# Kernel tuning notes

Hardware: AMD Instinct MI355X
Metric: run time of the kernel (lower is better)

## Reference

```python
import jax, jax.numpy as jnp
import numpy as np

C = 768; H = 12; D = C // H; R = 8; SCALE = 0.5; EPS = 1e-12
NEG = -1e9

def _lin(x, W, b):
    return x @ W + b

def _ln(x, g, b):
    m = jnp.mean(x, axis=-1, keepdims=True)
    v = jnp.mean((x - m) ** 2, axis=-1, keepdims=True)
    return (x - m) * jax.lax.rsqrt(v + EPS) * g + b

def setup_inputs() -> dict:
    key = jax.random.key(0)
    ks = jax.random.split(key, 16)
    B, T, K = 8, 512, 4
    s = 0.02
    inp = {
        'x': jax.random.normal(ks[0], (B, T, C), jnp.float32),
        'mask': jnp.ones((B, T), jnp.int32),
        'neighbour_rep': jax.random.normal(ks[1], (B, T - 1, K, C), jnp.float32),
        'Wq': jax.random.normal(ks[2], (C, C), jnp.float32) * s,
        'bq': jnp.zeros((C,), jnp.float32),
        'Wk': jax.random.normal(ks[3], (C, C), jnp.float32) * s,
        'bk': jnp.zeros((C,), jnp.float32),
        'Wv': jax.random.normal(ks[4], (C, C), jnp.float32) * s,
        'bv': jnp.zeros((C,), jnp.float32),
        'Wp': jax.random.normal(ks[5], (C, C), jnp.float32) * s,
        'bp': jnp.zeros((C,), jnp.float32),
        'Wd': jax.random.normal(ks[6], (C, R), jnp.float32) * s,
        'bd': jnp.zeros((R,), jnp.float32),
        'Wu': jax.random.normal(ks[7], (R, C), jnp.float32) * s,
        'bu': jnp.zeros((C,), jnp.float32),
        'ln_g': jnp.ones((C,), jnp.float32),
        'ln_b': jnp.zeros((C,), jnp.float32),
    }
    return inp

def _softmax_stable(att):
    # manual max-sub-exp-sum softmax, matching stable_softmax
    att = att - jnp.max(att, axis=-1, keepdims=True)
    att = jnp.exp(att)
    return att / jnp.sum(att, axis=-1, keepdims=True)

def _heads(t, n_tok):
    B = t.shape[0]
    return t.reshape(B, n_tok, H, D)

def reference(x, mask, neighbour_rep, Wq, bq, Wk, bk, Wv, bv, Wp, bp, Wd, bd, Wu, bu, ln_g, ln_b):
    B, T, _ = x.shape
    inv = 1.0 / jnp.sqrt(jnp.float32(D))
    mvalid = (mask != 0)[:, None, None, :]  # [B,1,1,T]

    # ---- self attention: queries are x[:,1:], keys/values over full seq ----
    q = _heads(_lin(x[:, 1:], Wq, bq), T - 1)      # [B,T-1,H,D]
    k = _heads(_lin(x, Wk, bk), T)                 # [B,T,H,D]
    v = _heads(_lin(x, Wv, bv), T)
    att = jnp.einsum('bqhd,bkhd->bhqk', q, k) * inv
    att = jnp.where(mvalid, att, NEG)
    att = _softmax_stable(att)
    y_self = jnp.einsum('bhqk,bkhd->bqhd', att, v).reshape(B, T - 1, C)
    y_self = _lin(y_self, Wp, bp)

    # ---- cls attention: single query (token 0), low-rank key projection ----
    qc = _heads(_lin(x[:, :1], Wq, bq), 1)                         # [B,1,H,D]
    kc = _heads(_lin(_lin(x, Wd, bd), Wu, bu), T)                  # [B,T,H,D]
    attc = jnp.einsum('bqhd,bkhd->bhqk', qc, kc) * inv
    attc = jnp.where(mvalid, attc, NEG)
    attc = _softmax_stable(attc)
    y_cls = jnp.einsum('bhqk,bkhd->bqhd', attc, v).reshape(B, 1, C)
    y_cls = _lin(y_cls, Wp, bp)

    # ---- neighbour attention over small candidate set per token ----
    cand = jnp.concatenate([x[:, 1:, None, :], neighbour_rep], axis=2)  # [B,T-1,Kc,C]
    Kc = cand.shape[2]
    qn = _lin(cand, Wq, bq).reshape(B, T - 1, Kc, H, D)
    kn = _lin(_lin(cand, Wd, bd), Wu, bu).reshape(B, T - 1, Kc, H, D)
    vn = _lin(cand, Wv, bv).reshape(B, T - 1, Kc, H, D)
    attn = jnp.einsum('btihd,btjhd->bthij', qn, kn) * inv
    attn = _softmax_stable(attn)
    out = jnp.einsum('bthij,btjhd->btihd', attn, vn).reshape(B, T - 1, Kc, C)
    out = _lin(out, Wp, bp)
    y_neigh = out[:, :, 0, :]
    neigh_tmp = out[:, :, 1:, :]

    y = SCALE * y_neigh + (1.0 - SCALE) * y_self
    neighbour_out = _ln(neigh_tmp + neighbour_rep, ln_g, ln_b)
    y = jnp.concatenate([y_cls, y], axis=1)
    y = _ln(y + x, ln_g, ln_b)
    return y, neighbour_out
```

## Files before the change

### kernel.cpp

```cpp
#include <hip/hip_runtime.h>
#include <math.h>

#define C_    768
#define H_    12
#define D_    64
#define B_    8
#define T_    512
#define TM1   511
#define R_    8
#define KN_   4
#define KC5   5
#define SCALE_ 0.5f
#define EPS_  1e-12f
#define NEG_  -1000000000.0f
#define INV_  0.125f
#define LDQ   2432
#define QPOFF 2304
#define LDVQ  896
#define NT_   4096
#define NRR_  16352

typedef __bf16 bf16_t;
typedef __bf16 bf16x4_t __attribute__((ext_vector_type(4)));
typedef __bf16 bf16x8_t __attribute__((ext_vector_type(8)));
typedef float  f32x4_t  __attribute__((ext_vector_type(4)));
typedef const void __attribute__((address_space(1)))* gas_t;
typedef void       __attribute__((address_space(3)))* las_t;

__device__ __forceinline__ void gl_lds16(const bf16_t* g, bf16_t* l) {
  __builtin_amdgcn_global_load_lds((gas_t)g, (las_t)l, 16, 0, 0);
}

__device__ __forceinline__ int swz(int row, int g) {
  return row * 32 + (((g ^ (row >> 1)) & 3) << 3);
}

struct GemmDesc {
  const bf16_t* A; int lda;
  const bf16_t* Bt;
  const float* bias;
  bf16_t* Cbf; int ldc;
  bf16_t* Ctr; int trcol0; int mode;
  int M, K, N, gx, nwg;
};

__global__ __launch_bounds__(256) void prep(
    const float* __restrict__ x, const float* __restrict__ nrep,
    const float* __restrict__ Wq, const float* __restrict__ Wk,
    const float* __restrict__ Wv, const float* __restrict__ Wp,
    const float* __restrict__ Wd, const float* __restrict__ Wu,
    const float* __restrict__ bq, const float* __restrict__ bk,
    const float* __restrict__ bv, const float* __restrict__ bu,
    const float* __restrict__ bp,
    bf16_t* __restrict__ xbf, bf16_t* __restrict__ nrbf,
    bf16_t* __restrict__ Wbig, bf16_t* __restrict__ Wtp,
    bf16_t* __restrict__ Wvbf,
    float* __restrict__ WdT, float* __restrict__ bbig,
    float* __restrict__ zb768)
{
  __shared__ float tile[32][33];
  const int bid = blockIdx.x, tid = threadIdx.x;
  if (bid < 1024) {
    const long n = (long)NT_ * C_;
    for (long i = ((long)bid * 256 + tid) * 4; i < n; i += (long)1024 * 256 * 4) {
      float4 v = *(const float4*)(x + i);
      bf16x4_t o = {(bf16_t)v.x, (bf16_t)v.y, (bf16_t)v.z, (bf16_t)v.w};
      *(bf16x4_t*)(xbf + i) = o;
    }
  } else if (bid < 3072) {
    const long n = (long)NRR_ * C_;
    for (long i = ((long)(bid - 1024) * 256 + tid) * 4; i < n;
         i += (long)2048 * 256 * 4) {
      float4 v = *(const float4*)(nrep + i);
      bf16x4_t o = {(bf16_t)v.x, (bf16_t)v.y, (bf16_t)v.z, (bf16_t)v.w};
      *(bf16x4_t*)(nrbf + i) = o;
    }
  } else if (bid < 5376) {
    int sub = bid - 3072;
    const int which = sub / 576; sub %= 576;
    if (which == 2) {
      const long i = ((long)sub * 256 + tid) * 4;
      float4 v = *(const float4*)(Wv + i);
      bf16x4_t o = {(bf16_t)v.x, (bf16_t)v.y, (bf16_t)v.z, (bf16_t)v.w};
      *(bf16x4_t*)(Wvbf + i) = o;
    } else {
      const float* W = which == 0 ? Wq : which == 1 ? Wk : Wp;
      bf16_t* Wt = (which == 3) ? Wtp : Wbig + (size_t)which * C_ * C_;
      const int n0 = (sub % 24) * 32, k0 = (sub / 24) * 32;
      const int tx = tid & 31, ty = tid >> 5;
      #pragma unroll
      for (int r = ty; r < 32; r += 8)
        tile[r][tx] = W[(size_t)(k0 + r) * C_ + n0 + tx];
      __syncthreads();
      #pragma unroll
      for (int r = ty; r < 32; r += 8)
        Wt[(size_t)(n0 + r) * C_ + k0 + tx] = (bf16_t)tile[tx][r];
    }
  } else if (bid < 5760) {
    const int idx = (bid - 5376) * 256 + tid;
    const int n = idx / C_, k = idx % C_;
    const int h = n / 10, r = n % 10;
    float s = 0.f;
    if (h < H_ && r < 9) {
      if (r < 8) {
        #pragma unroll 8
        for (int j = 0; j < 64; ++j)
          s += Wu[r * C_ + h * 64 + j] * Wq[(size_t)k * C_ + h * 64 + j];
      } else {
        #pragma unroll 8
        for (int j = 0; j < 64; ++j)
          s += bu[h * 64 + j] * Wq[(size_t)k * C_ + h * 64 + j];
      }
    }
    Wbig[(size_t)(QPOFF + n) * C_ + k] = (bf16_t)s;
  } else if (bid < 5784) {
    const int idx = (bid - 5760) * 256 + tid;
    if (idx < R_ * C_) {
      const int r = idx / C_, k = idx % C_;
      WdT[idx] = Wd[(size_t)k * R_ + r];
    }
  } else {
    const int i = (bid - 5784) * 256 + tid;
    if (i < LDQ) {
      float v;
      if (i < 768) v = bq[i];
      else if (i < 1536) v = bk[i - 768];
      else if (i < 2304) {
        const int n = i - 1536;
        float s = bp[n];
        for (int m = 0; m < C_; ++m) s += bv[m] * Wp[(size_t)m * C_ + n];
        v = s;
      } else {
        const int n = i - QPOFF, h = n / 10, r = n % 10;
        v = 0.f;
        if (h < H_ && r < 9) {
          if (r < 8) {
            float s = 0.f;
            for (int j = 0; j < 64; ++j) s += bq[h * 64 + j] * Wu[r * C_ + h * 64 + j];
            v = s;
          } else {
            float s = 0.f;
            for (int j = 0; j < 64; ++j) s += bq[h * 64 + j] * bu[h * 64 + j];
            v = s;
          }
        }
      }
      bbig[i] = v;
    } else if (i < LDQ + 768) {
      zb768[i - LDQ] = 0.f;
    }
  }
}

__device__ __forceinline__ void gemm_body(const GemmDesc& d, int bid0, char* pool)
{
  bf16_t* Cs = (bf16_t*)pool;

  int lid = bid0;
  {
    const int nwg = d.nwg;
    const int q0 = nwg >> 3, r0 = nwg & 7;
    const int xcd = lid & 7, idx = lid >> 3;
    lid = (xcd < r0 ? xcd * (q0 + 1) : r0 * (q0 + 1) + (xcd - r0) * q0) + idx;
  }
  const int row0 = (lid / d.gx) * 128;
  const int col0 = (lid % d.gx) * 128;

  const int tid = threadIdx.x;
  const int lane = tid & 63;
  const int wv = tid >> 6;
  const int wr = (wv >> 1) * 64;
  const int wc = (wv & 1) * 64;
  const int wvo = wv * 512;

  const int sr = tid >> 2;
  const int ssl = (tid & 3) ^ ((sr >> 1) & 3);
  const int sk = ssl * 8;

  int ra0 = row0 + sr;       if (ra0 > d.M - 1) ra0 = d.M - 1;
  int ra1 = row0 + 64 + sr;  if (ra1 > d.M - 1) ra1 = d.M - 1;
  const bf16_t* ga0 = d.A + (size_t)ra0 * d.lda + sk;
  const bf16_t* ga1 = d.A + (size_t)ra1 * d.lda + sk;
  const bf16_t* gb0 = d.Bt + (size_t)(col0 + sr) * d.K + sk;
  const bf16_t* gb1 = d.Bt + (size_t)(col0 + 64 + sr) * d.K + sk;

  f32x4_t acc[4][4];
  #pragma unroll
  for (int i = 0; i < 4; ++i)
    #pragma unroll
    for (int j = 0; j < 4; ++j) acc[i][j] = (f32x4_t){0.f, 0.f, 0.f, 0.f};

  const int fm = lane & 15;
  const int g = lane >> 4;

  {
    bf16_t* a0 = (bf16_t*)pool;
    bf16_t* b0 = (bf16_t*)(pool + 8192);
    gl_lds16(ga0, a0 + wvo);
    gl_lds16(ga1, a0 + 2048 + wvo);
    gl_lds16(gb0, b0 + wvo);
    gl_lds16(gb1, b0 + 2048 + wvo);
  }
  __syncthreads();

  unsigned cur = 0;
  for (int k0 = 32; k0 < d.K; k0 += 32) {
    {
      char* nb = pool + ((cur ^ 1u) << 14);
      bf16_t* na = (bf16_t*)nb;
      bf16_t* nbb = (bf16_t*)(nb + 8192);
      gl_lds16(ga0 + k0, na + wvo);
      gl_lds16(ga1 + k0, na + 2048 + wvo);
      gl_lds16(gb0 + k0, nbb + wvo);
      gl_lds16(gb1 + k0, nbb + 2048 + wvo);
    }
    {
      const bf16_t* cA = (const bf16_t*)(pool + (cur << 14));
      const bf16_t* cB = (const bf16_t*)(pool + (cur << 14) + 8192);
      bf16x8_t af[4], bfr[4];
      #pragma unroll
      for (int mi = 0; mi < 4; ++mi)
        af[mi] = *(const bf16x8_t*)(cA + swz(wr + mi * 16 + fm, g));
      #pragma unroll
      for (int ni = 0; ni < 4; ++ni)
        bfr[ni] = *(const bf16x8_t*)(cB + swz(wc + ni * 16 + fm, g));
      __builtin_amdgcn_s_setprio(1);
      #pragma unroll
      for (int mi = 0; mi < 4; ++mi)
        #pragma unroll
        for (int ni = 0; ni < 4; ++ni)
          acc[mi][ni] = __builtin_amdgcn_mfma_f32_16x16x32_bf16(af[mi], bfr[ni],
                                                                acc[mi][ni], 0, 0, 0);
      __builtin_amdgcn_s_setprio(0);
    }
    __syncthreads();
    cur ^= 1u;
  }
  {
    const bf16_t* cA = (const bf16_t*)(pool + (cur << 14));
    const bf16_t* cB = (const bf16_t*)(pool + (cur << 14) + 8192);
    bf16x8_t af[4], bfr[4];
    #pragma unroll
    for (int mi = 0; mi < 4; ++mi)
      af[mi] = *(const bf16x8_t*)(cA + swz(wr + mi * 16 + fm, g));
    #pragma unroll
    for (int ni = 0; ni < 4; ++ni)
      bfr[ni] = *(const bf16x8_t*)(cB + swz(wc + ni * 16 + fm, g));
    __builtin_amdgcn_s_setprio(1);
    #pragma unroll
    for (int mi = 0; mi < 4; ++mi)
      #pragma unroll
      for (int ni = 0; ni < 4; ++ni)
        acc[mi][ni] = __builtin_amdgcn_mfma_f32_16x16x32_bf16(af[mi], bfr[ni],
                                                              acc[mi][ni], 0, 0, 0);
    __builtin_amdgcn_s_setprio(0);
  }
  __syncthreads();

  const int r4 = (lane >> 4) * 4;

  if (d.mode & 2) {
    #pragma unroll
    for (int ni = 0; ni < 4; ++ni) {
      const int col = col0 + wc + ni * 16 + fm;
      if ((unsigned)(col - d.trcol0) < 768u) {
        const int vcol = col - d.trcol0;
        const float bv = d.bias[col];
        #pragma unroll
        for (int mi = 0; mi < 4; ++mi) {
          const int rb = row0 + wr + mi * 16 + r4;
          bf16x4_t o4 = {(bf16_t)(acc[mi][ni][0] + bv), (bf16_t)(acc[mi][ni][1] + bv),
                         (bf16_t)(acc[mi][ni][2] + bv), (bf16_t)(acc[mi][ni][3] + bv)};
          size_t idx = ((size_t)(rb >> 9) * H_ + (size_t)(vcol >> 6)) * ((size_t)D_ * T_)
                     + (size_t)(vcol & 63) * T_ + (size_t)(rb & 511);
          *(bf16x4_t*)(d.Ctr + idx) = o4;
        }
      }
    }
  }

  #pragma unroll
  for (int p = 0; p < 2; ++p) {
    if (wr == p * 64) {
      #pragma unroll
      for (int ni = 0; ni < 4; ++ni) {
        const int col = wc + ni * 16 + fm;
        const float bv = d.bias[col0 + col];
        #pragma unroll
        for (int mi = 0; mi < 4; ++mi) {
          const int lrow = mi * 16 + r4;
          #pragma unroll
          for (int r = 0; r < 4; ++r)
            Cs[(lrow + r) * 136 + col] = (bf16_t)(acc[mi][ni][r] + bv);
        }
      }
    }
    __syncthreads();
    const int rrow = tid >> 2;
    const int cc = (tid & 3) * 32;
    const int grow = row0 + p * 64 + rrow;
    if ((d.mode & 1) && grow < d.M) {
      bf16_t* gp = d.Cbf + (size_t)grow * d.ldc + col0 + cc;
      const bf16_t* lp = Cs + rrow * 136 + cc;
      #pragma unroll
      for (int j = 0; j < 4; ++j)
        *(bf16x8_t*)(gp + j * 8) = *(const bf16x8_t*)(lp + j * 8);
    }
    __syncthreads();
  }
}

__device__ __forceinline__ void gemv8w_body(
    const bf16_t* __restrict__ A, const float* __restrict__ WdT,
    const float* __restrict__ bd, float* __restrict__ out, int M, int bid)
{
  const int w = (int)threadIdx.x >> 6, lane = (int)threadIdx.x & 63;
  const int row0 = bid * 16 + w * 4;
  #pragma unroll
  for (int rr = 0; rr < 4; ++rr) {
    const int row = row0 + rr;
    if (row >= M) return;
    const bf16_t* ar = A + (size_t)row * C_ + lane * 12;
    float xv[12];
    #pragma unroll
    for (int c = 0; c < 3; ++c) {
      bf16x4_t v = *(const bf16x4_t*)(ar + c * 4);
      #pragma unroll
      for (int j = 0; j < 4; ++j) xv[c * 4 + j] = (float)v[j];
    }
    float acc[8];
    #pragma unroll
    for (int r = 0; r < 8; ++r) {
      const float* wr = WdT + r * C_ + lane * 12;
      float4 w0 = *(const float4*)(wr);
      float4 w1 = *(const float4*)(wr + 4);
      float4 w2 = *(const float4*)(wr + 8);
      acc[r] = xv[0]*w0.x + xv[1]*w0.y + xv[2]*w0.z + xv[3]*w0.w
             + xv[4]*w1.x + xv[5]*w1.y + xv[6]*w1.z + xv[7]*w1.w
             + xv[8]*w2.x + xv[9]*w2.y + xv[10]*w2.z + xv[11]*w2.w;
    }
    #pragma unroll
    for (int off = 32; off > 0; off >>= 1) {
      #pragma unroll
      for (int r = 0; r < 8; ++r) acc[r] += __shfl_xor(acc[r], off);
    }
    if (lane == 0) {
      #pragma unroll
      for (int r = 0; r < 8; ++r)
        out[(size_t)row * R_ + r] = acc[r] + bd[r];
    }
  }
}

__global__ __launch_bounds__(256) void mega1(
    GemmDesc d0, int n0, GemmDesc d1, int n1,
    const bf16_t* Ag1, const bf16_t* Ag2,
    const float* WdT, const float* bd,
    float* o1, int M1, int ng1, float* o2, int M2)
{
  __shared__ __align__(16) char pool[32768];
  int bid = blockIdx.x;
  if (bid < n0) { gemm_body(d0, bid, pool); return; }
  bid -= n0;
  if (bid < n1) { gemm_body(d1, bid, pool); return; }
  bid -= n1;
  if (bid < ng1) { gemv8w_body(Ag1, WdT, bd, o1, M1, bid); return; }
  bid -= ng1;
  gemv8w_body(Ag2, WdT, bd, o2, M2, bid);
}

__global__ __launch_bounds__(256) void gemm_mfma_k(GemmDesc d) {
  __shared__ __align__(16) char pool[32768];
  gemm_body(d, blockIdx.x, pool);
}

__device__ void attn_body(
    const bf16_t* __restrict__ QKVc, const bf16_t* __restrict__ Vtg,
    const int* __restrict__ mask, bf16_t* __restrict__ yout,
    char* pool, int bid)
{
  bf16_t* Ks   = (bf16_t*)pool;
  bf16_t* Vs   = (bf16_t*)(pool + 8192);
  bf16_t* Pl   = (bf16_t*)(pool + 16384);
  float* fac_s = (float*)(pool + 24576);
  float* l_s   = (float*)(pool + 24832);
  int*   msk_s = (int*)(pool + 25088);

  const int qt0 = (bid & 7) * 64;
  const int h = (bid >> 3) % H_;
  const int b = bid / 96;
  const int tid = threadIdx.x;
  const int lane = tid & 63;
  const int w = tid >> 6;
  const int lq = lane & 15;
  const int g = lane >> 4;

  const int qi_frag = qt0 + w * 16 + lq;
  const int qtok = (qi_frag < TM1 ? qi_frag : TM1 - 1) + 1;
  bf16x8_t qf[2];
  {
    const bf16_t* qp = QKVc + ((size_t)(b * T_) + qtok) * LDQ + h * D_ + 8 * g;
    qf[0] = *(const bf16x8_t*)qp;
    qf[1] = *(const bf16x8_t*)(qp + 32);
  }

  const bf16_t* kbase = QKVc + (size_t)(b * T_) * LDQ + 768 + h * D_;
  const bf16_t* vbase = Vtg + ((size_t)(b * H_) + h) * ((size_t)D_ * T_);

  f32x4_t o[4];
  #pragma unroll
  for (int i = 0; i < 4; ++i) o[i] = (f32x4_t){0.f, 0.f, 0.f, 0.f};
  float m = -INFINITY, l = 0.f;

  for (int kt = 0; kt < T_; kt += 64) {
    #pragma unroll
    for (int i = 0; i < 2; ++i) {
      const int tp = tid + i * 256;
      const int kr = tp >> 3;
      const int sl = tp & 7;
      const int ss = sl ^ (kr & 7);
      gl_lds16(kbase + (size_t)(kt + kr) * LDQ + 8 * ss,
               Ks + (size_t)(i * 4 + w) * 512);
      gl_lds16(vbase + (size_t)kr * T_ + kt + 8 * ss,
               Vs + (size_t)(i * 4 + w) * 512);
    }
    if (tid < 64) msk_s[tid] = mask[b * T_ + kt + tid];
    __syncthreads();

    f32x4_t st[4];
    __builtin_amdgcn_s_setprio(1);
    #pragma unroll
    for (int t = 0; t < 4; ++t) {
      st[t] = (f32x4_t){0.f, 0.f, 0.f, 0.f};
      const int kk = t * 16 + lq;
      const bf16_t* krow = Ks + kk * 64;
      bf16x8_t kf0 = *(const bf16x8_t*)(krow + 8 * ((g)     ^ (kk & 7)));
      bf16x8_t kf1 = *(const bf16x8_t*)(krow + 8 * ((4 + g) ^ (kk & 7)));
      st[t] = __builtin_amdgcn_mfma_f32_16x16x32_bf16(kf0, qf[0], st[t], 0, 0, 0);
      st[t] = __builtin_amdgcn_mfma_f32_16x16x32_bf16(kf1, qf[1], st[t], 0, 0, 0);
    }
    __builtin_amdgcn_s_setprio(0);

    float p[16];
    float mt = -INFINITY;
    #pragma unroll
    for (int t = 0; t < 4; ++t) {
      const int4 mk = *(const int4*)&msk_s[t * 16 + 4 * g];
      p[4*t+0] = mk.x ? st[t][0] * INV_ : NEG_;
      p[4*t+1] = mk.y ? st[t][1] * INV_ : NEG_;
      p[4*t+2] = mk.z ? st[t][2] * INV_ : NEG_;
      p[4*t+3] = mk.w ? st[t][3] * INV_ : NEG_;
      mt = fmaxf(mt, fmaxf(fmaxf(p[4*t], p[4*t+1]), fmaxf(p[4*t+2], p[4*t+3])));
    }
    mt = fmaxf(mt, __shfl_xor(mt, 16));
    mt = fmaxf(mt, __shfl_xor(mt, 32));
    const float mnew = fmaxf(m, mt);
    const float fac = __expf(m - mnew);
    float ps = 0.f;
    #pragma unroll
    for (int i = 0; i < 16; ++i) { p[i] = __expf(p[i] - mnew); ps += p[i]; }
    ps += __shfl_xor(ps, 16);
    ps += __shfl_xor(ps, 32);
    l = l * fac + ps;
    m = mnew;
    if (lane < 16) fac_s[w * 16 + lane] = fac;

    bf16_t* prow = Pl + w * 1024 + lq * 64;
    #pragma unroll
    for (int t = 0; t < 4; ++t) {
      bf16x4_t pb = {(bf16_t)p[4*t], (bf16_t)p[4*t+1],
                     (bf16_t)p[4*t+2], (bf16_t)p[4*t+3]};
      *(bf16x4_t*)(prow + 8 * ((2*t + (g >> 1)) ^ (lq & 7)) + 4 * (g & 1)) = pb;
    }
    bf16x8_t pa0 = *(const bf16x8_t*)(prow + 8 * ((g)     ^ (lq & 7)));
    bf16x8_t pa1 = *(const bf16x8_t*)(prow + 8 * ((4 + g) ^ (lq & 7)));

    const float4 fc = *(const float4*)&fac_s[w * 16 + 4 * g];
    __builtin_amdgcn_s_setprio(1);
    #pragma unroll
    for (int db = 0; db < 4; ++db) {
      const int dr = db * 16 + lq;
      const bf16_t* vrow = Vs + dr * 64;
      bf16x8_t vf0 = *(const bf16x8_t*)(vrow + 8 * ((g)     ^ (dr & 7)));
      bf16x8_t vf1 = *(const bf16x8_t*)(vrow + 8 * ((4 + g) ^ (dr & 7)));
      o[db][0] *= fc.x; o[db][1] *= fc.y; o[db][2] *= fc.z; o[db][3] *= fc.w;
      o[db] = __builtin_amdgcn_mfma_f32_16x16x32_bf16(pa0, vf0, o[db], 0, 0, 0);
      o[db] = __builtin_amdgcn_mfma_f32_16x16x32_bf16(pa1, vf1, o[db], 0, 0, 0);
    }
    __builtin_amdgcn_s_setprio(0);
    __syncthreads();
  }

  if (lane < 16) l_s[w * 16 + lane] = l;
  const float4 lv = *(const float4*)&l_s[w * 16 + 4 * g];
  const float rl0 = 1.f / lv.x, rl1 = 1.f / lv.y;
  const float rl2 = 1.f / lv.z, rl3 = 1.f / lv.w;
  const int qr0 = qt0 + w * 16 + 4 * g;
  #pragma unroll
  for (int db = 0; db < 4; ++db) {
    const int col = h * D_ + db * 16 + lq;
    bf16_t* yp = yout + ((size_t)(b * TM1) + qr0) * C_ + col;
    if (qr0 + 0 < TM1) yp[0 * (size_t)C_] = (bf16_t)(o[db][0] * rl0);
    if (qr0 + 1 < TM1) yp[1 * (size_t)C_] = (bf16_t)(o[db][1] * rl1);
    if (qr0 + 2 < TM1) yp[2 * (size_t)C_] = (bf16_t)(o[db][2] * rl2);
    if (qr0 + 3 < TM1) yp[3 * (size_t)C_] = (bf16_t)(o[db][3] * rl3);
  }
}

__device__ void cls_body(
    const bf16_t* __restrict__ QKVc, const float* __restrict__ t1,
    const int* __restrict__ mask, float* __restrict__ ycp,
    char* pool, int cbid)
{
  float* Vs   = (float*)pool;
  float* Ps   = (float*)(pool + 16640);
  float* qp_s = (float*)(pool + 16960);

  const int b = cbid / H_, h = cbid % H_;
  const int tid = threadIdx.x;
  const int lane = tid & 63;

  if (tid < 9)
    qp_s[tid] = (float)QKVc[(size_t)(b * T_) * LDQ + QPOFF + h * 10 + tid];
  __syncthreads();

  float m = -INFINITY, l = 0.f, acc = 0.f, mnew = 0.f;
  for (int kt = 0; kt < T_; kt += 64) {
    for (int rr = tid >> 6; rr < 64; rr += 4)
      Vs[rr * 65 + lane] =
          (float)QKVc[((size_t)(b * T_) + kt + rr) * LDQ + 1536 + h * D_ + lane];
    __syncthreads();
    if (tid < 64) {
      const float* t1r = t1 + ((size_t)(b * T_) + kt + tid) * R_;
      float sc = qp_s[8];
      #pragma unroll
      for (int r = 0; r < 8; ++r) sc += qp_s[r] * t1r[r];
      sc *= INV_;
      if (!mask[b * T_ + kt + tid]) sc = NEG_;
      float mt = sc;
      #pragma unroll
      for (int off = 32; off > 0; off >>= 1) mt = fmaxf(mt, __shfl_xor(mt, off));
      mnew = fmaxf(m, mt);
      float e = __expf(sc - mnew);
      float ssum = e;
      #pragma unroll
      for (int off = 32; off > 0; off >>= 1) ssum += __shfl_xor(ssum, off);
      float fac = __expf(m - mnew);
      acc *= fac;
      l = l * fac + ssum;
      Ps[tid] = e;
    }
    __syncthreads();
    if (tid < 64) {
      #pragma unroll
      for (int j = 0; j < 64; ++j) acc += Ps[j] * Vs[j * 65 + tid];
      m = mnew;
    }
    __syncthreads();
  }
  if (tid < 64) ycp[(size_t)b * C_ + h * D_ + tid] = acc / l;
}

__global__ __launch_bounds__(256) void attn_cls(
    const bf16_t* __restrict__ QKVc, const bf16_t* __restrict__ Vtg,
    const int* __restrict__ mask, bf16_t* __restrict__ yout,
    const float* __restrict__ t1, float* __restrict__ ycp)
{
  __shared__ __align__(16) char pool[25344];
  const int bid = blockIdx.x;
  if (bid < 768) attn_body(QKVc, Vtg, mask, yout, pool, bid);
  else           cls_body(QKVc, t1, mask, ycp, pool, bid - 768);
}

__global__ __launch_bounds__(256) void neigh_attn(
    const bf16_t* __restrict__ QKVc, const float* __restrict__ t1,
    const bf16_t* __restrict__ vqn, const float* __restrict__ t2,
    const bf16_t* __restrict__ ysp, int b0, bf16_t* __restrict__ poutn)
{
  __shared__ float vs[KC5 * C_];
  __shared__ float qp_s[KC5][128];
  __shared__ float t2_s[KC5][8];
  __shared__ float Ps[H_ * 25];

  const int tid = threadIdx.x;
  const int bt = blockIdx.x;
  const int bb = bt / TM1, t = bt % TM1;
  const int b = b0 + bb;
  const size_t tok = (size_t)(b * T_) + t + 1;
  const size_t nrow = ((size_t)(bb * TM1) + t) * KN_;

  for (int idx = tid; idx < KC5 * 96; idx += 256) {
    int i = idx / 96, d8 = (idx % 96) * 8;
    const bf16_t* vp = (i == 0) ? QKVc + tok * LDQ + 1536 + d8
                                : vqn + (nrow + i - 1) * LDVQ + d8;
    bf16x8_t vv = *(const bf16x8_t*)vp;
    #pragma unroll
    for (int j = 0; j < 8; ++j) vs[i * C_ + d8 + j] = (float)vv[j];
  }
  for (int idx = tid; idx < KC5 * 16; idx += 256) {
    int i = idx / 16, c8 = (idx % 16) * 8;
    const bf16_t* qpp = (i == 0) ? QKVc + tok * LDQ + QPOFF + c8
                                 : vqn + (nrow + i - 1) * LDVQ + 768 + c8;
    bf16x8_t qv = *(const bf16x8_t*)qpp;
    #pragma unroll
    for (int j = 0; j < 8; ++j) qp_s[i][c8 + j] = (float)qv[j];
  }
  if (tid < KC5 * 8) {
    int i = tid / 8, r = tid & 7;
    t2_s[i][r] = (i == 0) ? t1[tok * R_ + r] : t2[(nrow + i - 1) * R_ + r];
  }
  __syncthreads();

  if (tid < H_ * KC5) {
    int h = tid / KC5, i = tid % KC5;
    float sc[KC5];
    #pragma unroll
    for (int j = 0; j < KC5; ++j) {
      float s = qp_s[i][h * 10 + 8];
      #pragma unroll
      for (int r = 0; r < 8; ++r) s += qp_s[i][h * 10 + r] * t2_s[j][r];
      sc[j] = s * INV_;
    }
    float mt = sc[0];
    #pragma unroll
    for (int j = 1; j < KC5; ++j) mt = fmaxf(mt, sc[j]);
    float e[KC5], ssum = 0.f;
    #pragma unroll
    for (int j = 0; j < KC5; ++j) { e[j] = __expf(sc[j] - mt); ssum += e[j]; }
    float rs = 1.f / ssum;
    #pragma unroll
    for (int j = 0; j < KC5; ++j) Ps[h * 25 + i * KC5 + j] = e[j] * rs;
  }
  __syncthreads();

  const bf16_t* ysrow = ysp + ((size_t)(b * TM1) + t) * C_;
  for (int idx = tid; idx < KC5 * C_; idx += 256) {
    int i = idx / C_, c = idx % C_;
    int h = c / D_;
    float sum = 0.f;
    #pragma unroll
    for (int j = 0; j < KC5; ++j)
      sum += Ps[h * 25 + i * KC5 + j] * vs[j * C_ + c];
    if (i == 0) sum = SCALE_ * sum + (1.f - SCALE_) * (float)ysrow[c];
    poutn[(((size_t)(bb * TM1) + t) * KC5 + i) * C_ + c] = (bf16_t)sum;
  }
}

__device__ __forceinline__ void block_reduce2(float& s, float& ss, float* red) {
  #pragma unroll
  for (int off = 32; off > 0; off >>= 1) {
    s += __shfl_down(s, off);
    ss += __shfl_down(ss, off);
  }
  int wid = threadIdx.x >> 6;
  if ((threadIdx.x & 63) == 0) { red[wid * 2] = s; red[wid * 2 + 1] = ss; }
  __syncthreads();
  s  = red[0] + red[2] + red[4] + red[6];
  ss = red[1] + red[3] + red[5] + red[7];
}

__device__ __forceinline__ void ln_row(const float vals[3], float s, float ss,
                                       const float* __restrict__ g,
                                       const float* __restrict__ bb,
                                       float* __restrict__ orow, float* red) {
  block_reduce2(s, ss, red);
  float mean = s * (1.f / (float)C_);
  float var = ss * (1.f / (float)C_) - mean * mean;
  var = fmaxf(var, 0.f);
  float rs = rsqrtf(var + EPS_);
  #pragma unroll
  for (int ii = 0; ii < 3; ++ii) {
    int c = threadIdx.x + ii * 256;
    orow[c] = (vals[ii] - mean) * rs * g[c] + bb[c];
  }
}

__global__ __launch_bounds__(256) void combine_all(
    const bf16_t* __restrict__ poutnb, const float* __restrict__ x,
    const float* __restrict__ g, const float* __restrict__ bln,
    int b0, float* __restrict__ dout, float* __restrict__ dout1,
    const bf16_t* __restrict__ nrcbf, int nMain,
    const float* __restrict__ ycp)
{
  __shared__ float red[8];
  int bid = blockIdx.x;
  float vals[3], s = 0.f, ss = 0.f;
  if (bid < nMain) {
    const int bbb = bid / TM1, t = bid % TM1;
    const int b = b0 + bbb;
    const bf16_t* pn = poutnb + (((size_t)(bbb * TM1) + t) * KC5 + 0) * C_;
    const float* xr = x + ((size_t)(b * T_) + t + 1) * C_;
    float* orow = dout + ((size_t)(b * T_) + t + 1) * C_;
    #pragma unroll
    for (int ii = 0; ii < 3; ++ii) {
      int c = threadIdx.x + ii * 256;
      float v = (float)pn[c] + xr[c];
      vals[ii] = v; s += v; ss += v * v;
    }
    ln_row(vals, s, ss, g, bln, orow, red);
    return;
  }
  bid -= nMain;
  if (bid < nMain * KN_) {
    const int i1 = bid % KN_;
    const int bt = bid / KN_;
    const int bbb = bt / TM1, t = bt % TM1;
    const int b = b0 + bbb;
    const bf16_t* pn = poutnb + ((size_t)bt * KC5 + 1 + i1) * C_;
    const bf16_t* nr = nrcbf + ((size_t)bt * KN_ + i1) * C_;
    float* orow = dout1 + (((size_t)(b * TM1) + t) * KN_ + i1) * C_;
    #pragma unroll
    for (int ii = 0; ii < 3; ++ii) {
      int c = threadIdx.x + ii * 256;
      float v = (float)pn[c] + (float)nr[c];
      vals[ii] = v; s += v; ss += v * v;
    }
    ln_row(vals, s, ss, g, bln, orow, red);
    return;
  }
  bid -= nMain * KN_;
  const int b = bid;
  const float* yc = ycp + (size_t)b * C_;
  const float* xr = x + (size_t)(b * T_) * C_;
  float* orow = dout + (size_t)(b * T_) * C_;
  #pragma unroll
  for (int ii = 0; ii < 3; ++ii) {
    int c = threadIdx.x + ii * 256;
    float v = yc[c] + xr[c];
    vals[ii] = v; s += v; ss += v * v;
  }
  ln_row(vals, s, ss, g, bln, orow, red);
}

extern "C" void kernel_launch(void* const* d_in, const int* in_sizes, int n_in,
                              void* d_out, int out_size, void* d_ws, size_t ws_size,
                              hipStream_t stream) {
  (void)in_sizes; (void)n_in; (void)out_size;
  const float* x    = (const float*)d_in[0];
  const int*   mask = (const int*)d_in[1];
  const float* nrep = (const float*)d_in[2];
  const float* Wq = (const float*)d_in[3];  const float* bq = (const float*)d_in[4];
  const float* Wk = (const float*)d_in[5];  const float* bk = (const float*)d_in[6];
  const float* Wv = (const float*)d_in[7];  const float* bv = (const float*)d_in[8];
  const float* Wp = (const float*)d_in[9];  const float* bp = (const float*)d_in[10];
  const float* Wd = (const float*)d_in[11]; const float* bd = (const float*)d_in[12];
  const float* Wu = (const float*)d_in[13]; const float* bu = (const float*)d_in[14];
  const float* lng = (const float*)d_in[15];
  const float* lnb = (const float*)d_in[16];
  float* dout = (float*)d_out;
  const size_t OUT1 = (size_t)B_ * T_ * C_;

  char* ws = (char*)d_ws;
  size_t off = 0;
  auto alloc = [&](size_t bytes) -> void* {
    void* p = ws + off; off += (bytes + 255) & ~(size_t)255; return p;
  };
  const size_t NT = (size_t)NT_;
  const size_t NR = (size_t)NRR_;
  const size_t YSROWS = (size_t)B_ * TM1;

  bf16_t* xbf   = (bf16_t*)alloc(NT * C_ * 2);
  bf16_t* nrbf  = (bf16_t*)alloc(NR * C_ * 2);
  bf16_t* Wbig  = (bf16_t*)alloc((size_t)LDQ * C_ * 2);
  bf16_t* Wtp   = (bf16_t*)alloc((size_t)C_ * C_ * 2);
  bf16_t* Wvbf  = (bf16_t*)alloc((size_t)C_ * C_ * 2);
  float*  WdT   = (float*)alloc((size_t)R_ * C_ * 4);
  float*  bbig  = (float*)alloc(LDQ * 4);
  float*  zb768 = (float*)alloc(768 * 4);
  bf16_t* QKVc  = (bf16_t*)alloc(NT * LDQ * 2);
  bf16_t* Vtg   = (bf16_t*)alloc(NT * C_ * 2);
  float*  t1    = (float*)alloc(NT * R_ * 4);
  bf16_t* ysp   = (bf16_t*)alloc(YSROWS * C_ * 2);
  float*  ycp   = (float*)alloc((size_t)B_ * C_ * 4);
  const size_t fixed = off;
  const size_t perb = (size_t)TM1 * KN_ * LDVQ * 2
                    + (size_t)TM1 * KN_ * R_ * 4
                    + (size_t)TM1 * KC5 * C_ * 2 + 4 * 256;
  int nb = 1;
  for (int cand : {8, 4, 2, 1}) {
    if (fixed + perb * (size_t)cand <= ws_size) { nb = cand; break; }
  }
  bf16_t* poutnb = (bf16_t*)alloc((size_t)nb * TM1 * KC5 * C_ * 2);
  bf16_t* vqn  = (bf16_t*)alloc((size_t)nb * TM1 * KN_ * LDVQ * 2);
  float*  t2   = (float*)alloc((size_t)nb * TM1 * KN_ * R_ * 4);

  dim3 blk(256);

  prep<<<5797, blk, 0, stream>>>(x, nrep, Wq, Wk, Wv, Wp, Wd, Wu,
                                 bq, bk, bv, bu, bp,
                                 xbf, nrbf, Wbig, Wtp, Wvbf, WdT, bbig, zb768);

  GemmDesc dwvp;
  dwvp.A = Wtp; dwvp.lda = C_; dwvp.Bt = Wvbf; dwvp.bias = zb768;
  dwvp.Cbf = Wbig + (size_t)1536 * C_; dwvp.ldc = C_;
  dwvp.Ctr = nullptr; dwvp.trcol0 = 0; dwvp.mode = 1;
  dwvp.M = C_; dwvp.K = C_; dwvp.N = C_; dwvp.gx = 6; dwvp.nwg = 36;
  gemm_mfma_k<<<36, blk, 0, stream>>>(dwvp);

  GemmDesc dqkv;
  dqkv.A = xbf; dqkv.lda = C_; dqkv.Bt = Wbig; dqkv.bias = bbig;
  dqkv.Cbf = QKVc; dqkv.ldc = LDQ; dqkv.Ctr = Vtg; dqkv.trcol0 = 1536;
  dqkv.mode = 3; dqkv.M = (int)NT; dqkv.K = C_; dqkv.N = LDQ;
  dqkv.gx = LDQ / 128; dqkv.nwg = (LDQ / 128) * 32;

  bool first = true;
  for (int b0 = 0; b0 < B_; b0 += nb) {
    const int Mn = nb * TM1 * KN_;
    const bf16_t* nrcbf = nrbf + (size_t)b0 * TM1 * KN_ * C_;

    GemmDesc dvqn;
    dvqn.A = nrcbf; dvqn.lda = C_; dvqn.Bt = Wbig + (size_t)1536 * C_;
    dvqn.bias = bbig + 1536; dvqn.Cbf = vqn; dvqn.ldc = LDVQ;
    dvqn.Ctr = nullptr; dvqn.trcol0 = 0; dvqn.mode = 1;
    dvqn.M = Mn; dvqn.K = C_; dvqn.N = LDVQ;
    dvqn.gx = LDVQ / 128; dvqn.nwg = (LDVQ / 128) * ((Mn + 127) / 128);

    const int n0 = first ? dqkv.nwg : 0;
    const int M1 = first ? (int)NT : 0;
    const int ng1 = first ? (int)((NT + 15) / 16) : 0;
    const int ng2 = (Mn + 15) / 16;

    mega1<<<n0 + dvqn.nwg + ng1 + ng2, blk, 0, stream>>>(
        dqkv, n0, dvqn, dvqn.nwg, xbf, nrcbf, WdT, bd, t1, M1, ng1, t2, Mn);

    if (first) {
      attn_cls<<<768 + 96, blk, 0, stream>>>(QKVc, Vtg, mask, ysp, t1, ycp);
    }

    neigh_attn<<<nb * TM1, blk, 0, stream>>>(QKVc, t1, vqn, t2, ysp, b0, poutnb);

    combine_all<<<nb * TM1 * (1 + KN_) + (first ? 8 : 0), blk, 0, stream>>>(
        poutnb, x, lng, lnb, b0, dout, dout + OUT1, nrcbf, nb * TM1, ycp);

    first = false;
  }
}
```

Before: 236.8 us.

## Merge self/cls attention and neighbour attention into one launch

Fuses the attn_cls and neigh_attn kernels into a single attn_neigh launch that dispatches blocks by index range, sharing one shared-memory pool. To remove the dependency of neighbour attention on the self-attention output, the SCALE blend with y_self moves from neigh_attn into combine_all. This saves a kernel launch and lets the two attention workloads run concurrently. In exchange, neighbour blocks now use the larger 25 KB pool, which may lower their occupancy.

```diff
diff --git a/kernel.cpp b/kernel.cpp
--- a/kernel.cpp
+++ b/kernel.cpp
@@ -561,29 +561,17 @@
   if (tid < 64) ycp[(size_t)b * C_ + h * D_ + tid] = acc / l;
 }
 
-__global__ __launch_bounds__(256) void attn_cls(
-    const bf16_t* __restrict__ QKVc, const bf16_t* __restrict__ Vtg,
-    const int* __restrict__ mask, bf16_t* __restrict__ yout,
-    const float* __restrict__ t1, float* __restrict__ ycp)
-{
-  __shared__ __align__(16) char pool[25344];
-  const int bid = blockIdx.x;
-  if (bid < 768) attn_body(QKVc, Vtg, mask, yout, pool, bid);
-  else           cls_body(QKVc, t1, mask, ycp, pool, bid - 768);
-}
-
-__global__ __launch_bounds__(256) void neigh_attn(
+__device__ void neigh_body(
     const bf16_t* __restrict__ QKVc, const float* __restrict__ t1,
     const bf16_t* __restrict__ vqn, const float* __restrict__ t2,
-    const bf16_t* __restrict__ ysp, int b0, bf16_t* __restrict__ poutn)
+    int b0, bf16_t* __restrict__ poutn, char* pool, int bt)
 {
-  __shared__ float vs[KC5 * C_];
-  __shared__ float qp_s[KC5][128];
-  __shared__ float t2_s[KC5][8];
-  __shared__ float Ps[H_ * 25];
+  float* vs   = (float*)pool;
+  float* qp_s = (float*)(pool + 15360);
+  float* t2_s = (float*)(pool + 17920);
+  float* Ps   = (float*)(pool + 18080);
 
   const int tid = threadIdx.x;
-  const int bt = blockIdx.x;
   const int bb = bt / TM1, t = bt % TM1;
   const int b = b0 + bb;
   const size_t tok = (size_t)(b * T_) + t + 1;
@@ -603,11 +591,11 @@
                                  : vqn + (nrow + i - 1) * LDVQ + 768 + c8;
     bf16x8_t qv = *(const bf16x8_t*)qpp;
     #pragma unroll
-    for (int j = 0; j < 8; ++j) qp_s[i][c8 + j] = (float)qv[j];
+    for (int j = 0; j < 8; ++j) qp_s[i * 128 + c8 + j] = (float)qv[j];
   }
   if (tid < KC5 * 8) {
     int i = tid / 8, r = tid & 7;
-    t2_s[i][r] = (i == 0) ? t1[tok * R_ + r] : t2[(nrow + i - 1) * R_ + r];
+    t2_s[i * 8 + r] = (i == 0) ? t1[tok * R_ + r] : t2[(nrow + i - 1) * R_ + r];
   }
   __syncthreads();
 
@@ -616,9 +604,9 @@
     float sc[KC5];
     #pragma unroll
     for (int j = 0; j < KC5; ++j) {
-      float s = qp_s[i][h * 10 + 8];
-      #pragma unroll
-      for (int r = 0; r < 8; ++r) s += qp_s[i][h * 10 + r] * t2_s[j][r];
+      float s = qp_s[i * 128 + h * 10 + 8];
+      #pragma unroll
+      for (int r = 0; r < 8; ++r) s += qp_s[i * 128 + h * 10 + r] * t2_s[j * 8 + r];
       sc[j] = s * INV_;
     }
     float mt = sc[0];
@@ -633,7 +621,6 @@
   }
   __syncthreads();
 
-  const bf16_t* ysrow = ysp + ((size_t)(b * TM1) + t) * C_;
   for (int idx = tid; idx < KC5 * C_; idx += 256) {
     int i = idx / C_, c = idx % C_;
     int h = c / D_;
@@ -641,9 +628,25 @@
     #pragma unroll
     for (int j = 0; j < KC5; ++j)
       sum += Ps[h * 25 + i * KC5 + j] * vs[j * C_ + c];
-    if (i == 0) sum = SCALE_ * sum + (1.f - SCALE_) * (float)ysrow[c];
     poutn[(((size_t)(bb * TM1) + t) * KC5 + i) * C_ + c] = (bf16_t)sum;
   }
+}
+
+__global__ __launch_bounds__(256) void attn_neigh(
+    int nAttn, int nCls,
+    const bf16_t* __restrict__ QKVc, const bf16_t* __restrict__ Vtg,
+    const int* __restrict__ mask, bf16_t* __restrict__ ysp,
+    const float* __restrict__ t1, float* __restrict__ ycp,
+    const bf16_t* __restrict__ vqn, const float* __restrict__ t2,
+    int b0, bf16_t* __restrict__ poutn)
+{
+  __shared__ __align__(16) char pool[25344];
+  int bid = blockIdx.x;
+  if (bid < nAttn) { attn_body(QKVc, Vtg, mask, ysp, pool, bid); return; }
+  bid -= nAttn;
+  if (bid < nCls) { cls_body(QKVc, t1, mask, ycp, pool, bid); return; }
+  bid -= nCls;
+  neigh_body(QKVc, t1, vqn, t2, b0, poutn, pool, bid);
 }
 
 __device__ __forceinline__ void block_reduce2(float& s, float& ss, float* red) {
@@ -676,7 +679,8 @@
 }
 
 __global__ __launch_bounds__(256) void combine_all(
-    const bf16_t* __restrict__ poutnb, const float* __restrict__ x,
+    const bf16_t* __restrict__ poutnb, const bf16_t* __restrict__ ysp,
+    const float* __restrict__ x,
     const float* __restrict__ g, const float* __restrict__ bln,
     int b0, float* __restrict__ dout, float* __restrict__ dout1,
     const bf16_t* __restrict__ nrcbf, int nMain,
@@ -689,12 +693,13 @@
     const int bbb = bid / TM1, t = bid % TM1;
     const int b = b0 + bbb;
     const bf16_t* pn = poutnb + (((size_t)(bbb * TM1) + t) * KC5 + 0) * C_;
+    const bf16_t* ys = ysp + ((size_t)(b * TM1) + t) * C_;
     const float* xr = x + ((size_t)(b * T_) + t + 1) * C_;
     float* orow = dout + ((size_t)(b * T_) + t + 1) * C_;
     #pragma unroll
     for (int ii = 0; ii < 3; ++ii) {
       int c = threadIdx.x + ii * 256;
-      float v = (float)pn[c] + xr[c];
+      float v = SCALE_ * (float)pn[c] + (1.f - SCALE_) * (float)ys[c] + xr[c];
       vals[ii] = v; s += v; ss += v * v;
     }
     ln_row(vals, s, ss, g, bln, orow, red);
@@ -823,14 +828,13 @@
     mega1<<<n0 + dvqn.nwg + ng1 + ng2, blk, 0, stream>>>(
         dqkv, n0, dvqn, dvqn.nwg, xbf, nrcbf, WdT, bd, t1, M1, ng1, t2, Mn);
 
-    if (first) {
-      attn_cls<<<768 + 96, blk, 0, stream>>>(QKVc, Vtg, mask, ysp, t1, ycp);
-    }
-
-    neigh_attn<<<nb * TM1, blk, 0, stream>>>(QKVc, t1, vqn, t2, ysp, b0, poutnb);
+    const int nAttn = first ? 768 : 0;
+    const int nCls  = first ? 96 : 0;
+    attn_neigh<<<nAttn + nCls + nb * TM1, blk, 0, stream>>>(
+        nAttn, nCls, QKVc, Vtg, mask, ysp, t1, ycp, vqn, t2, b0, poutnb);
 
     combine_all<<<nb * TM1 * (1 + KN_) + (first ? 8 : 0), blk, 0, stream>>>(
-        poutnb, x, lng, lnb, b0, dout, dout + OUT1, nrcbf, nb * TM1, ycp);
+        poutnb, ysp, x, lng, lnb, b0, dout, dout + OUT1, nrcbf, nb * TM1, ycp);
 
     first = false;
   }
```

Result: faster. 223.1 us (-5.8%).
